# Optimization experiments

Measured on AMD Instinct MI355X. Metric: run time of the kernel, lower is better.

The kernel has to match this reference:

```python
import jax, jax.numpy as jnp
import numpy as np

NUM_HEADS = 16
HEAD_CH = 64
D_MODEL = 1024  # == NUM_HEADS*HEAD_CH -> out_mapper is Identity


def setup_inputs() -> dict:
    key = jax.random.key(0)
    k1, k2, k3 = jax.random.split(key, 3)
    tokens = jax.random.normal(k1, (2, 2048, D_MODEL), dtype=jnp.float32)
    w_qkv = jax.random.normal(k2, (D_MODEL, 3 * D_MODEL), dtype=jnp.float32) * (1.0 / np.sqrt(D_MODEL))
    b_qkv = jax.random.normal(k3, (3 * D_MODEL,), dtype=jnp.float32) * 0.02
    return {"tokens": tokens, "w_qkv": w_qkv, "b_qkv": b_qkv}


def reference(tokens, w_qkv, b_qkv):
    b, n, _ = tokens.shape
    qkv = tokens @ w_qkv + b_qkv  # [b, n, 3*inner]
    q, k, v = jnp.split(qkv, 3, axis=-1)

    def heads(x):  # [b, n, h*d] -> [b, h, n, d]
        return x.reshape(b, n, NUM_HEADS, HEAD_CH).transpose(0, 2, 1, 3)

    q, k, v = heads(q), heads(k), heads(v)
    scores = jnp.einsum('bhqd,bhkd->bhqk', q, k) / jnp.sqrt(jnp.float32(HEAD_CH))
    attn = jax.nn.softmax(scores, axis=-1)
    out = jnp.einsum('bhqk,bhkd->bhqd', attn, v)  # [b, h, n, d]
    out = out.transpose(0, 2, 1, 3).reshape(b, n, NUM_HEADS * HEAD_CH)
    return out  # out_mapper is Identity since inner_channels == input_channels
```

## Files before the change

### kernel.cpp

```cpp
#include <hip/hip_runtime.h>
#include <stdint.h>

typedef __attribute__((ext_vector_type(8))) short shortx8;
typedef __attribute__((ext_vector_type(4))) float floatx4;
typedef unsigned short bf16_t;

#define NH 16
#define HD 64
#define SEQ 2048
#define BATCH 2
#define DM 1024
#define DM3 3072

#define GLDS(gp, lp) __builtin_amdgcn_global_load_lds( \
    (const __attribute__((address_space(1))) unsigned int*)(gp), \
    (__attribute__((address_space(3))) unsigned int*)(lp), 16, 0, 0)

#define BARX() __builtin_amdgcn_s_barrier()
#define VMCNT(n) asm volatile("s_waitcnt vmcnt(" #n ")" ::: "memory")
#define LGKM0() do { asm volatile("s_waitcnt lgkmcnt(0)" ::: "memory"); \
                     __builtin_amdgcn_sched_barrier(0); } while (0)

__device__ __forceinline__ bf16_t f2bf(float f) {
    unsigned int u = __float_as_uint(f);
    u += 0x7fff + ((u >> 16) & 1);
    return (bf16_t)(u >> 16);
}
__device__ __forceinline__ unsigned pk2bf(float lo, float hi) {
    return (unsigned)f2bf(lo) | ((unsigned)f2bf(hi) << 16);
}

__global__ __launch_bounds__(256) void conv_all(const float* __restrict__ tokens,
                                                bf16_t* __restrict__ tok_bf,
                                                const float* __restrict__ w,
                                                bf16_t* __restrict__ wt) {
    __shared__ bf16_t t[64 * 65];
    const int bx = blockIdx.x, tid = threadIdx.x;
    if (bx < 2048) {
        int idx = bx * 256 + tid;
        float4 a = ((const float4*)tokens)[idx * 2];
        float4 b = ((const float4*)tokens)[idx * 2 + 1];
        uint4 o;
        o.x = pk2bf(a.x, a.y);
        o.y = pk2bf(a.z, a.w);
        o.z = pk2bf(b.x, b.y);
        o.w = pk2bf(b.z, b.w);
        ((uint4*)tok_bf)[idx] = o;
    } else {
        const int bw = bx - 2048;
        const int n0 = (bw % 48) * 64, k0 = (bw / 48) * 64;
        for (int i = 0; i < 16; i++) {
            int idx = i * 256 + tid;
            int r = idx >> 6, c = idx & 63;
            t[r * 65 + c] = f2bf(w[(k0 + r) * DM3 + n0 + c]);
        }
        __syncthreads();
#pragma unroll
        for (int i = 0; i < 2; i++) {
            int idx = i * 256 + tid;
            int r = idx >> 3, g = idx & 7;
            union { unsigned short s[8]; uint4 v; } u;
#pragma unroll
            for (int j = 0; j < 8; j++) u.s[j] = t[(g * 8 + j) * 65 + r];
            *(uint4*)&wt[(n0 + r) * DM + k0 + g * 8] = u.v;
        }
    }
}


#define QSCALE 0.18033688011f

__device__ __forceinline__ void stage_half(const bf16_t* __restrict__ g0,
                                           bf16_t* lds) {
    GLDS(g0, lds);
    GLDS(g0 + (size_t)64 * DM, lds + 4096);
}

template<int MH>
__device__ __forceinline__ void rd_a(const bf16_t* As, int slot, int arow,
                                     int kg0, int kg1, shortx8 (&af)[4][2]) {
#pragma unroll
    for (int t = 0; t < 4; t++) {
        const bf16_t* p = &As[slot * 16384 + arow + (MH * 4 + t) * 2048];
        af[t][0] = *(const shortx8*)(p + kg0);
        af[t][1] = *(const shortx8*)(p + kg1);
    }
}

template<int NHH>
__device__ __forceinline__ void rd_b(const bf16_t* Bs, int slot, int brow,
                                     int kg0, int kg1, shortx8 (&bfr)[4][2]) {
#pragma unroll
    for (int t = 0; t < 2; t++) {
        const bf16_t* p = &Bs[slot * 16384 + brow + (NHH * 2 + t) * 4096];
        bfr[NHH * 2 + t][0] = *(const shortx8*)(p + kg0);
        bfr[NHH * 2 + t][1] = *(const shortx8*)(p + kg1);
    }
}

template<bool SW, int MH, int NHH>
__device__ __forceinline__ void mfmaq(const shortx8 (&af)[4][2], const shortx8 (&bfr)[4][2],
                                      floatx4 (&acc)[8][4]) {
    __builtin_amdgcn_s_setprio(1);
#pragma unroll
    for (int i = 0; i < 4; i++)
#pragma unroll
        for (int j = 0; j < 2; j++) {
#pragma unroll
            for (int ks = 0; ks < 2; ks++)
                acc[MH * 4 + i][NHH * 2 + j] = SW
                    ? __builtin_amdgcn_mfma_f32_16x16x32_bf16(bfr[NHH * 2 + j][ks], af[i][ks],
                                                              acc[MH * 4 + i][NHH * 2 + j], 0, 0, 0)
                    : __builtin_amdgcn_mfma_f32_16x16x32_bf16(af[i][ks], bfr[NHH * 2 + j][ks],
                                                              acc[MH * 4 + i][NHH * 2 + j], 0, 0, 0);
        }
    __builtin_amdgcn_s_setprio(0);
}

template<bool SW>
__device__ __forceinline__ void kloop256(const bf16_t* __restrict__ A,
                                         const bf16_t* __restrict__ Bt,
                                         char* smem, int m0, int n0,
                                         floatx4 (&acc)[8][4]) {
    const int tid = threadIdx.x;
    const int lane = tid & 63, wave = tid >> 6;
    const int wr = wave >> 2, wc = wave & 3;
    const int quad = lane >> 4, l16 = lane & 15;
    const int h3 = l16 & 7;
    bf16_t* As = (bf16_t*)smem;
    bf16_t* Bs = (bf16_t*)(smem + 65536);
    const int srow = tid >> 3;
    const int sg8 = ((tid & 7) ^ (srow & 7)) * 8;
    const bf16_t* Ag = A + (size_t)(m0 + srow) * DM + sg8;
    const bf16_t* Bg = Bt + (size_t)(n0 + srow) * DM + sg8;

    const int kg0 = (quad ^ h3) * 8;
    const int kg1 = ((4 + quad) ^ h3) * 8;
    const int arow = (wr * 16 + l16) * 64;
    const int brow = (wc * 16 + l16) * 64;

    shortx8 af[4][2], bfr[4][2];

    stage_half(Ag,                            &As[tid * 8]);
    stage_half(Bg,                            &Bs[tid * 8]);
    stage_half(Ag + (size_t)128 * DM,         &As[8192 + tid * 8]);
    stage_half(Bg + (size_t)128 * DM,         &Bs[8192 + tid * 8]);
    stage_half(Ag + 64,                       &As[16384 + tid * 8]);
    stage_half(Bg + 64,                       &Bs[16384 + tid * 8]);
    VMCNT(8);
    BARX();

    for (int t = 0; t < 16; ++t) {
        const int s = t & 1;
        const int t1 = (t + 1) & 15, t2 = (t + 2) & 15;
        rd_a<0>(As, s, arow, kg0, kg1, af);
        rd_b<0>(Bs, s, brow, kg0, kg1, bfr);
        stage_half(Ag + (size_t)128 * DM + t1 * 64, &As[(s ^ 1) * 16384 + 8192 + tid * 8]);
        VMCNT(6);
        BARX(); LGKM0();
        mfmaq<SW, 0, 0>(af, bfr, acc);
        BARX();
        rd_b<1>(Bs, s, brow, kg0, kg1, bfr);
        stage_half(Bg + (size_t)128 * DM + t1 * 64, &Bs[(s ^ 1) * 16384 + 8192 + tid * 8]);
        BARX(); LGKM0();
        mfmaq<SW, 0, 1>(af, bfr, acc);
        BARX();
        rd_a<1>(As, s, arow, kg0, kg1, af);
        stage_half(Ag + t2 * 64, &As[s * 16384 + tid * 8]);
        BARX(); LGKM0();
        mfmaq<SW, 1, 0>(af, bfr, acc);
        BARX();
        stage_half(Bg + t2 * 64, &Bs[s * 16384 + tid * 8]);
        VMCNT(8);
        BARX();
        mfmaq<SW, 1, 1>(af, bfr, acc);
        BARX();
    }
}

__global__ __launch_bounds__(512, 2) void qkv_gemm(const bf16_t* __restrict__ A,
                                                   const bf16_t* __restrict__ Bt,
                                                   const float* __restrict__ bias,
                                                   bf16_t* __restrict__ Qo,
                                                   bf16_t* __restrict__ Ko,
                                                   bf16_t* __restrict__ Vto) {
    __shared__ __align__(16) char smem[131072];
    const int m0 = blockIdx.x * 256;
    const int n0 = blockIdx.y * 256;
    const int tid = threadIdx.x;
    const int lane = tid & 63, wave = tid >> 6;
    const int wr = wave >> 2, wc = wave & 3;
    const int quad = lane >> 4, l16 = lane & 15;
    const int part = n0 >> 10;
    const int b = m0 >> 11, pos0 = m0 & 2047;
    floatx4 acc[8][4] = {};

    if (part != 2) {
        kloop256<true>(A, Bt, smem, m0, n0, acc);
        asm volatile("s_waitcnt vmcnt(0)" ::: "memory");
        __syncthreads();
        bf16_t* Cs = (bf16_t*)smem;
#pragma unroll
        for (int mf = 0; mf < 8; mf++) {
            int m = wr * 16 + mf * 32 + l16;
            char* rowp = (char*)Cs + m * 512;
            int sw = (m & 7) << 4;
#pragma unroll
            for (int nf = 0; nf < 4; nf++) {
                int n = wc * 16 + nf * 64 + quad * 4;
                float4 bv = *(const float4*)&bias[n0 + n];
                float v0 = acc[mf][nf][0] + bv.x, v1 = acc[mf][nf][1] + bv.y;
                float v2 = acc[mf][nf][2] + bv.z, v3 = acc[mf][nf][3] + bv.w;
                if (part == 0) { v0 *= QSCALE; v1 *= QSCALE; v2 *= QSCALE; v3 *= QSCALE; }
                uint2 pk;
                pk.x = pk2bf(v0, v1);
                pk.y = pk2bf(v2, v3);
                *(uint2*)(rowp + ((n * 2) ^ sw)) = pk;
            }
        }
        __syncthreads();
        bf16_t* dst = (part == 0) ? Qo : Ko;
#pragma unroll
        for (int it = 0; it < 16; it++) {
            int c = it * 512 + tid;
            int m = c >> 5, g = c & 31;
            uint4 v = *(const uint4*)((char*)Cs + m * 512 + ((g * 16) ^ ((m & 7) << 4)));
            int ng = n0 + g * 8;
            int h = (ng >> 6) & 15, d = ng & 63;
            *(uint4*)&dst[(size_t)((b * NH + h) * SEQ + pos0 + m) * HD + d] = v;
        }
    } else {
        kloop256<false>(A, Bt, smem, m0, n0, acc);
        asm volatile("s_waitcnt vmcnt(0)" ::: "memory");
        __syncthreads();
        bf16_t* Cs = (bf16_t*)smem;
#pragma unroll
        for (int nf = 0; nf < 4; nf++) {
            int n = wc * 16 + nf * 64 + l16;
            float bv = bias[n0 + n];
            char* rowp = (char*)Cs + n * 512;
            int sw = (n & 7) << 4;
#pragma unroll
            for (int mf = 0; mf < 8; mf++) {
                int m = wr * 16 + mf * 32 + quad * 4;
                uint2 pk;
                pk.x = pk2bf(acc[mf][nf][0] + bv, acc[mf][nf][1] + bv);
                pk.y = pk2bf(acc[mf][nf][2] + bv, acc[mf][nf][3] + bv);
                *(uint2*)(rowp + ((m * 2) ^ sw)) = pk;
            }
        }
        __syncthreads();
#pragma unroll
        for (int it = 0; it < 16; it++) {
            int c = it * 512 + tid;
            int n = c >> 5, g = c & 31;
            uint4 v = *(const uint4*)((char*)Cs + n * 512 + ((g * 16) ^ ((n & 7) << 4)));
            int ng = n0 + n;
            int h = (ng >> 6) & 15, d = ng & 63;
            *(uint4*)&Vto[(size_t)((b * NH + h) * HD + d) * SEQ + pos0 + g * 8] = v;
        }
    }
}

__global__ __launch_bounds__(256, 2) void attn(const bf16_t* __restrict__ Q,
                                               const bf16_t* __restrict__ K,
                                               const bf16_t* __restrict__ Vt,
                                               float* __restrict__ out) {
    __shared__ __align__(16) char smem[65536];
    bf16_t* Ks = (bf16_t*)smem;
    bf16_t* Vs = (bf16_t*)(smem + 16384);
    bf16_t* Ps = (bf16_t*)(smem + 32768);

    const int bh = blockIdx.x;
    const int qt_blk = blockIdx.y;
    const int b = bh >> 4, h = bh & 15;
    const int q0 = qt_blk * 128;
    const bf16_t* Qb = Q + ((size_t)bh * SEQ + q0) * HD;
    const bf16_t* Kb = K + (size_t)bh * SEQ * HD;
    const bf16_t* Vb = Vt + (size_t)bh * HD * SEQ;
    const int tid = threadIdx.x;
    const int wave = tid >> 6, lane = tid & 63;
    const int quad = lane >> 4, l16 = lane & 15;
    const int h3 = l16 & 7;
    const int qh = wave >> 1, kh = wave & 1;
    bf16_t* Pw = Ps + wave * 4096;

    const int srow = tid >> 3;
    const int sg8 = ((tid & 7) ^ (srow & 7)) * 8;
    const int vrow = tid >> 4;
    const int vg8 = (((tid & 15) ^ vrow) & 15) * 8;

    shortx8 qf[4][2];
    for (int qt = 0; qt < 4; qt++)
        for (int kc = 0; kc < 2; kc++)
            qf[qt][kc] = *(const shortx8*)&Qb[(qh * 64 + qt * 16 + l16) * 64 + kc * 32 + quad * 8];

    shortx8 ones;
    for (int i = 0; i < 8; i++) ones[i] = (short)0x3F80;

    const floatx4 minit = {-12.f, -12.f, -12.f, -12.f};
    floatx4 acc_l[4] = {};
    floatx4 acc_o[4][4] = {};

    for (int rr = 0; rr < 4; rr++) {
        GLDS(&Kb[(rr * 32 + srow) * 64 + sg8], &Ks[rr * 2048 + tid * 8]);
        GLDS(&Vb[(size_t)(rr * 16 + vrow) * SEQ + vg8], &Vs[rr * 2048 + tid * 8]);
    }
    __syncthreads();

    for (int it = 0; it < SEQ / 128; ++it) {
        shortx8 kf[2][4], vf[2][4];
        for (int kc = 0; kc < 2; kc++) {
            const int g = ((kc * 4 + quad) ^ h3) * 8;
            for (int kt = 0; kt < 4; kt++)
                kf[kc][kt] = *(const shortx8*)&Ks[(kh * 64 + kt * 16 + l16) * 64 + g];
        }
        for (int hp = 0; hp < 2; hp++)
            for (int dt = 0; dt < 4; dt++)
                vf[hp][dt] = *(const shortx8*)&Vs[(dt * 16 + l16) * 128 +
                                                  (((kh * 8 + hp * 4 + quad) ^ l16) & 15) * 8];
        __syncthreads();
        if (it + 1 < SEQ / 128) {
            const int kk = (it + 1) * 128;
            for (int rr = 0; rr < 4; rr++) {
                GLDS(&Kb[(kk + rr * 32 + srow) * 64 + sg8], &Ks[rr * 2048 + tid * 8]);
                GLDS(&Vb[(size_t)(rr * 16 + vrow) * SEQ + kk + vg8], &Vs[rr * 2048 + tid * 8]);
            }
        }

        for (int hp = 0; hp < 2; hp++) {
            floatx4 s[2][4];
            for (int k2 = 0; k2 < 2; k2++)
                for (int qt = 0; qt < 4; qt++) s[k2][qt] = minit;
            for (int kc = 0; kc < 2; kc++)
                for (int k2 = 0; k2 < 2; k2++)
                    for (int qt = 0; qt < 4; qt++)
                        s[k2][qt] = __builtin_amdgcn_mfma_f32_16x16x32_bf16(
                            kf[kc][hp * 2 + k2], qf[qt][kc], s[k2][qt], 0, 0, 0);
            for (int qt = 0; qt < 4; qt++)
                for (int k2 = 0; k2 < 2; k2++) {
                    unsigned u[4];
                    for (int r = 0; r < 4; r++)
                        u[r] = __float_as_uint(__builtin_amdgcn_exp2f(s[k2][qt][r])) + 0x8000u;
                    uint2 pk;
                    pk.x = __builtin_amdgcn_perm(u[1], u[0], 0x07060302u);
                    pk.y = __builtin_amdgcn_perm(u[3], u[2], 0x07060302u);
                    *(uint2*)&Pw[(qt * 16 + l16) * 64 +
                                 (((hp * 2 + k2) * 2 + (quad >> 1)) ^ h3) * 8 + (quad & 1) * 4] = pk;
                }
            const int gp = ((hp * 4 + quad) ^ h3) * 8;
            for (int qt = 0; qt < 4; qt++) {
                shortx8 pf = *(const shortx8*)&Pw[(qt * 16 + l16) * 64 + gp];
                acc_l[qt] = __builtin_amdgcn_mfma_f32_16x16x32_bf16(ones, pf, acc_l[qt], 0, 0, 0);
                for (int dt = 0; dt < 4; dt++)
                    acc_o[dt][qt] = __builtin_amdgcn_mfma_f32_16x16x32_bf16(vf[hp][dt], pf, acc_o[dt][qt], 0, 0, 0);
            }
        }
        __syncthreads();
    }

    float* Osh = (float*)smem;
    float* ml = (float*)(smem + 32768);
    if (kh == 1) {
        for (int qt = 0; qt < 4; qt++) {
            for (int dt = 0; dt < 4; dt++) {
                float4 o;
                o.x = acc_o[dt][qt][0]; o.y = acc_o[dt][qt][1];
                o.z = acc_o[dt][qt][2]; o.w = acc_o[dt][qt][3];
                *(float4*)&Osh[qh * 4096 + (qt * 16 + l16) * 64 +
                               (((dt * 4 + quad) ^ l16) & 15) * 4] = o;
            }
            if (quad == 0) ml[(qh * 4 + qt) * 16 + l16] = acc_l[qt][0];
        }
    }
    __syncthreads();
    if (kh == 0) {
        for (int qt = 0; qt < 4; qt++) {
            float l1 = ml[(qh * 4 + qt) * 16 + l16];
            float inv = 1.0f / (acc_l[qt][0] + l1);
            int q = q0 + qh * 64 + qt * 16 + l16;
            for (int dt = 0; dt < 4; dt++) {
                float4 o1 = *(const float4*)&Osh[qh * 4096 + (qt * 16 + l16) * 64 +
                                                 (((dt * 4 + quad) ^ l16) & 15) * 4];
                float4 o;
                o.x = (acc_o[dt][qt][0] + o1.x) * inv;
                o.y = (acc_o[dt][qt][1] + o1.y) * inv;
                o.z = (acc_o[dt][qt][2] + o1.z) * inv;
                o.w = (acc_o[dt][qt][3] + o1.w) * inv;
                *(float4*)&out[(size_t)(b * SEQ + q) * DM + h * HD + dt * 16 + quad * 4] = o;
            }
        }
    }
}

extern "C" void kernel_launch(void* const* d_in, const int* in_sizes, int n_in,
                              void* d_out, int out_size, void* d_ws, size_t ws_size,
                              hipStream_t stream) {
    const float* tokens = (const float*)d_in[0];
    const float* w = (const float*)d_in[1];
    const float* bias = (const float*)d_in[2];
    float* out = (float*)d_out;
    char* ws = (char*)d_ws;

    bf16_t* tok_bf = (bf16_t*)(ws);
    bf16_t* wt_bf  = (bf16_t*)(ws + (size_t)8 * 1024 * 1024);
    bf16_t* Qb     = (bf16_t*)(ws + (size_t)14 * 1024 * 1024);
    bf16_t* Kb     = (bf16_t*)(ws + (size_t)22 * 1024 * 1024);
    bf16_t* Vb     = (bf16_t*)(ws + (size_t)30 * 1024 * 1024);

    conv_all<<<2816, 256, 0, stream>>>(tokens, tok_bf, w, wt_bf);
    qkv_gemm<<<dim3(16, 12), 512, 0, stream>>>(tok_bf, wt_bf, bias, Qb, Kb, Vb);
    attn<<<dim3(32, 16), 256, 0, stream>>>(Qb, Kb, Vb, out);
}
```

Measured before the change: 156.8 us.

## Remap QKV GEMM blocks per XCD and batch all QK^T MFMAs before softmax

The QKV GEMM grid index is remapped so that consecutive blocks dispatched round-robin to the same XCD cover a compact 4x6 tile region, which improves L2 reuse of A and B panels within each XCD. In the attention kernel, the QK^T score computation for both half-tiles is issued as one batch before the exp/pack stage, with explicit full unrolling, giving the scheduler longer independent MFMA chains. The cost is higher register pressure from holding twice as many score accumulators, which could cause spills or reduce occupancy.

```diff
diff --git a/kernel.cpp b/kernel.cpp
--- a/kernel.cpp
+++ b/kernel.cpp
@@ -185,8 +185,10 @@
                                                    bf16_t* __restrict__ Ko,
                                                    bf16_t* __restrict__ Vto) {
     __shared__ __align__(16) char smem[131072];
-    const int m0 = blockIdx.x * 256;
-    const int n0 = blockIdx.y * 256;
+    const int id = blockIdx.y * 16 + blockIdx.x;
+    const int xcd = id & 7, k = id >> 3;
+    const int m0 = (((xcd & 3) * 4) + (k & 3)) * 256;
+    const int n0 = (((xcd >> 2) * 6) + (k >> 2)) * 256;
     const int tid = threadIdx.x;
     const int lane = tid & 63, wave = tid >> 6;
     const int wr = wave >> 2, wc = wave & 3;
@@ -328,30 +330,49 @@
             }
         }
 
-        for (int hp = 0; hp < 2; hp++) {
-            floatx4 s[2][4];
+        floatx4 s[2][2][4];
+#pragma unroll
+        for (int hp = 0; hp < 2; hp++)
+#pragma unroll
             for (int k2 = 0; k2 < 2; k2++)
-                for (int qt = 0; qt < 4; qt++) s[k2][qt] = minit;
-            for (int kc = 0; kc < 2; kc++)
+#pragma unroll
+                for (int qt = 0; qt < 4; qt++) s[hp][k2][qt] = minit;
+#pragma unroll
+        for (int kc = 0; kc < 2; kc++)
+#pragma unroll
+            for (int hp = 0; hp < 2; hp++)
+#pragma unroll
                 for (int k2 = 0; k2 < 2; k2++)
+#pragma unroll
                     for (int qt = 0; qt < 4; qt++)
-                        s[k2][qt] = __builtin_amdgcn_mfma_f32_16x16x32_bf16(
-                            kf[kc][hp * 2 + k2], qf[qt][kc], s[k2][qt], 0, 0, 0);
+                        s[hp][k2][qt] = __builtin_amdgcn_mfma_f32_16x16x32_bf16(
+                            kf[kc][hp * 2 + k2], qf[qt][kc], s[hp][k2][qt], 0, 0, 0);
+
+#pragma unroll
+        for (int hp = 0; hp < 2; hp++)
+#pragma unroll
             for (int qt = 0; qt < 4; qt++)
+#pragma unroll
                 for (int k2 = 0; k2 < 2; k2++) {
                     unsigned u[4];
+#pragma unroll
                     for (int r = 0; r < 4; r++)
-                        u[r] = __float_as_uint(__builtin_amdgcn_exp2f(s[k2][qt][r])) + 0x8000u;
+                        u[r] = __float_as_uint(__builtin_amdgcn_exp2f(s[hp][k2][qt][r])) + 0x8000u;
                     uint2 pk;
                     pk.x = __builtin_amdgcn_perm(u[1], u[0], 0x07060302u);
                     pk.y = __builtin_amdgcn_perm(u[3], u[2], 0x07060302u);
                     *(uint2*)&Pw[(qt * 16 + l16) * 64 +
                                  (((hp * 2 + k2) * 2 + (quad >> 1)) ^ h3) * 8 + (quad & 1) * 4] = pk;
                 }
+
+#pragma unroll
+        for (int hp = 0; hp < 2; hp++) {
             const int gp = ((hp * 4 + quad) ^ h3) * 8;
+#pragma unroll
             for (int qt = 0; qt < 4; qt++) {
                 shortx8 pf = *(const shortx8*)&Pw[(qt * 16 + l16) * 64 + gp];
                 acc_l[qt] = __builtin_amdgcn_mfma_f32_16x16x32_bf16(ones, pf, acc_l[qt], 0, 0, 0);
+#pragma unroll
                 for (int dt = 0; dt < 4; dt++)
                     acc_o[dt][qt] = __builtin_amdgcn_mfma_f32_16x16x32_bf16(vf[hp][dt], pf, acc_o[dt][qt], 0, 0, 0);
             }
```

Measured after the change: 158.9 us. Within noise of the previous version (+1.3%).
